# Kernel optimization log

Measured on AMD Instinct MI355X. Metric: run time of the kernel, lower is better.

Reference implementation:

```python
import jax, jax.numpy as jnp
import numpy as np

COMMITMENT_COST = 0.25


def setup_inputs() -> dict:
    key = jax.random.key(0)
    kx, ke = jax.random.split(key)
    x = jax.random.normal(kx, (16, 2048, 256), dtype=jnp.float32)
    embedding = jax.random.normal(ke, (4096, 256), dtype=jnp.float32)
    return {"x": x, "embedding": embedding}


def reference(x, embedding):
    # x: [B, T, D], embedding: [M, D]. Eval-mode VQ-EMA forward (no buffer updates).
    B, T, D = x.shape
    M = embedding.shape[0]
    x_flat = x.reshape(-1, D)  # [N, D], N = B*T

    distances = (
        jnp.sum(embedding * embedding, axis=1)[None, :]
        + jnp.sum(x_flat * x_flat, axis=1, keepdims=True)
        - 2.0 * (x_flat @ embedding.T)
    )
    indices = jnp.argmin(distances.astype(jnp.float32), axis=-1)  # [N]
    quantized = embedding[indices].reshape(x.shape)  # gather lookup, [B, T, D]

    # commitment loss, masked by nonpadding frames
    e_latent = (x - jax.lax.stop_gradient(quantized)) ** 2  # mse, reduction='none'
    nonpadding = (jnp.abs(x).sum(-1) > 0).astype(x.dtype)  # [B, T]
    e_latent_loss = (e_latent.mean(-1) * nonpadding).sum() / nonpadding.sum()
    loss = COMMITMENT_COST * e_latent_loss

    # straight-through estimator
    quantized_st = x + jax.lax.stop_gradient(quantized - x)

    # perplexity from code usage histogram (avoid materializing [N, M] one-hot)
    counts = jnp.zeros((M,), jnp.float32).at[indices].add(1.0)
    avg_probs = counts / indices.shape[0]
    perplexity = jnp.exp(-jnp.sum(avg_probs * jnp.log(avg_probs + 1e-10)))

    return quantized_st, loss, indices.reshape(B, T), perplexity
```

## Files before the change

### kernel.cpp

```cpp
#include <hip/hip_runtime.h>
#include <math.h>
#include <stdint.h>

#define D 256
#define N 32768
#define M 4096

#define LOSS_OFF 8388608
#define IDX_OFF  8388609
#define PERP_OFF 8421377

typedef _Float16 f16;
typedef _Float16 f16x8 __attribute__((ext_vector_type(8)));
typedef _Float16 f16x4 __attribute__((ext_vector_type(4)));
typedef float f32x4 __attribute__((ext_vector_type(4)));

#define WS_XH     0u
#define WS_XL     16777216u
#define WS_EH     33554432u
#define WS_EL     35651584u
#define WS_ENORM  37748736u
#define WS_COUNTS 37765120u
#define WS_IDX    37781504u
#define WS_CAND   37912576u
#define WS_LPART  38961152u
#define WS_NPART  38969344u
#define WS_NEEDED 38977536u
#define C_BLOCKS  2048

__device__ __forceinline__ void gload16(const void* g, void* l) {
    __builtin_amdgcn_global_load_lds(
        (const __attribute__((address_space(1))) uint32_t*)g,
        (__attribute__((address_space(3))) uint32_t*)l, 16, 0, 0);
}

__global__ __launch_bounds__(256) void init_kernel(const float* __restrict__ emb,
                                                   float* __restrict__ enorm,
                                                   unsigned* __restrict__ counts) {
    int tid = threadIdx.x;
    int lane = tid & 63;
    int wid = tid >> 6;
    int m = blockIdx.x * 4 + wid;
    const float4* e4 = (const float4*)(emb + (size_t)m * D);
    float4 v = e4[lane];
    float s = v.x * v.x + v.y * v.y + v.z * v.z + v.w * v.w;
    #pragma unroll
    for (int off = 32; off; off >>= 1) s += __shfl_xor(s, off);
    if (lane == 0) enorm[m] = s;
    int gid = blockIdx.x * 256 + tid;
    if (gid < M) counts[gid] = 0u;
}

__global__ __launch_bounds__(256) void convert_kernel(const float* __restrict__ s,
                                                      f16* __restrict__ dh,
                                                      f16* __restrict__ dl, int n4) {
    int i = blockIdx.x * 256 + threadIdx.x;
    if (i >= n4) return;
    float4 v = ((const float4*)s)[i];
    f16 h0 = (f16)v.x, h1 = (f16)v.y, h2 = (f16)v.z, h3 = (f16)v.w;
    f16 l0 = (f16)(v.x - (float)h0), l1 = (f16)(v.y - (float)h1);
    f16 l2 = (f16)(v.z - (float)h2), l3 = (f16)(v.w - (float)h3);
    f16x4 hv; hv[0] = h0; hv[1] = h1; hv[2] = h2; hv[3] = h3;
    f16x4 lv; lv[0] = l0; lv[1] = l1; lv[2] = l2; lv[3] = l3;
    *(f16x4*)(dh + (size_t)i * 4) = hv;
    *(f16x4*)(dl + (size_t)i * 4) = lv;
}

__global__ __launch_bounds__(256) void argmin_mfma(
    const f16* __restrict__ xh, const f16* __restrict__ xl,
    const f16* __restrict__ eh, const f16* __restrict__ el,
    const float* __restrict__ enorm, float2* __restrict__ cand)
{
    __shared__ f16 Als[2][128][64];
    __shared__ f16 Bls[2][128][64];
    __shared__ float2 msm[2][64];

    int tid = threadIdx.x;
    int lane = tid & 63;
    int wid = tid >> 6;
    int wr = wid >> 1, wc = wid & 1;
    int rb = blockIdx.x >> 2;
    int cs = blockIdx.x & 3;
    int row0 = rb * 128;

    int srow = lane >> 3;
    int sk = (((lane & 7) ^ srow) * 8);

    int rxor = lane & 7;

    float bestv[4][4];
    int bestc[4][4];
    #pragma unroll
    for (int i = 0; i < 4; ++i)
        #pragma unroll
        for (int r = 0; r < 4; ++r) { bestv[i][r] = 3.4e38f; bestc[i][r] = 0; }

    for (int ct = 0; ct < 8; ++ct) {
        int c0 = (cs * 8 + ct) * 128;
        f32x4 acc[4][4];
        #pragma unroll
        for (int i = 0; i < 4; ++i)
            #pragma unroll
            for (int j = 0; j < 4; ++j) acc[i][j] = (f32x4)0.0f;

        for (int kt = 0; kt < 4; ++kt) {
            int k0 = kt * 64;
            __syncthreads();
            #pragma unroll
            for (int q = 0; q < 4; ++q) {
                int ch = wid * 4 + q;
                int tr = ch * 8 + srow;
                size_t aoff = (size_t)(row0 + tr) * D + k0 + sk;
                size_t boff = (size_t)(c0 + tr) * D + k0 + sk;
                gload16(xh + aoff, (char*)&Als[0][0][0] + ch * 1024);
                gload16(xl + aoff, (char*)&Als[1][0][0] + ch * 1024);
                gload16(eh + boff, (char*)&Bls[0][0][0] + ch * 1024);
                gload16(el + boff, (char*)&Bls[1][0][0] + ch * 1024);
            }
            __syncthreads();

            #pragma unroll
            for (int ks = 0; ks < 2; ++ks) {
                int slot = ks * 4 + (lane >> 4);
                int sw = ((slot ^ rxor) * 8);
                int ar = wr * 64 + (lane & 15);
                int br = wc * 64 + (lane & 15);
                f16x8 ah[4], al[4], bh[4], bl[4];
                #pragma unroll
                for (int i = 0; i < 4; ++i) {
                    ah[i] = *(const f16x8*)&Als[0][ar + i * 16][sw];
                    al[i] = *(const f16x8*)&Als[1][ar + i * 16][sw];
                }
                #pragma unroll
                for (int j = 0; j < 4; ++j) {
                    bh[j] = *(const f16x8*)&Bls[0][br + j * 16][sw];
                    bl[j] = *(const f16x8*)&Bls[1][br + j * 16][sw];
                }
                #pragma unroll
                for (int i = 0; i < 4; ++i)
                    #pragma unroll
                    for (int j = 0; j < 4; ++j)
                        acc[i][j] = __builtin_amdgcn_mfma_f32_16x16x32_f16(
                            ah[i], bh[j], acc[i][j], 0, 0, 0);
                #pragma unroll
                for (int i = 0; i < 4; ++i)
                    #pragma unroll
                    for (int j = 0; j < 4; ++j)
                        acc[i][j] = __builtin_amdgcn_mfma_f32_16x16x32_f16(
                            ah[i], bl[j], acc[i][j], 0, 0, 0);
                #pragma unroll
                for (int i = 0; i < 4; ++i)
                    #pragma unroll
                    for (int j = 0; j < 4; ++j)
                        acc[i][j] = __builtin_amdgcn_mfma_f32_16x16x32_f16(
                            al[i], bh[j], acc[i][j], 0, 0, 0);
            }
        }
        float enj[4];
        #pragma unroll
        for (int j = 0; j < 4; ++j) enj[j] = enorm[c0 + wc * 64 + j * 16 + (lane & 15)];
        #pragma unroll
        for (int i = 0; i < 4; ++i)
            #pragma unroll
            for (int j = 0; j < 4; ++j) {
                int c = c0 + wc * 64 + j * 16 + (lane & 15);
                #pragma unroll
                for (int r = 0; r < 4; ++r) {
                    float s = enj[j] - 2.0f * acc[i][j][r];
                    if (s < bestv[i][r]) { bestv[i][r] = s; bestc[i][r] = c; }
                }
            }
    }

    float rv[4][4]; int rc[4][4];
    #pragma unroll
    for (int i = 0; i < 4; ++i)
        #pragma unroll
        for (int r = 0; r < 4; ++r) {
            float v = bestv[i][r]; int c = bestc[i][r];
            #pragma unroll
            for (int off = 8; off; off >>= 1) {
                float ov = __shfl_xor(v, off);
                int oc = __shfl_xor(c, off);
                if (ov < v || (ov == v && oc < c)) { v = ov; c = oc; }
            }
            rv[i][r] = v; rc[i][r] = c;
            if ((lane & 15) == 0 && wc == 1) {
                int rloc = i * 16 + (lane >> 4) * 4 + r;
                float2 p; p.x = v; p.y = __int_as_float(c);
                msm[wr][rloc] = p;
            }
        }
    __syncthreads();
    if (wc == 0 && (lane & 15) == 0) {
        #pragma unroll
        for (int i = 0; i < 4; ++i)
            #pragma unroll
            for (int r = 0; r < 4; ++r) {
                int rloc = i * 16 + (lane >> 4) * 4 + r;
                float v = rv[i][r]; int c = rc[i][r];
                float2 o = msm[wr][rloc];
                float ov = o.x; int oc = __float_as_int(o.y);
                if (ov < v || (ov == v && oc < c)) { v = ov; c = oc; }
                float2 p; p.x = v; p.y = __int_as_float(c);
                cand[(size_t)cs * N + row0 + wr * 64 + rloc] = p;
            }
    }
}

__global__ __launch_bounds__(256) void merge_kernel(const float2* __restrict__ cand,
                                                    unsigned* __restrict__ counts,
                                                    int* __restrict__ idx_out,
                                                    float* __restrict__ idx_f) {
    int row = blockIdx.x * 256 + threadIdx.x;
    float bv = 3.4e38f; int bc = 0;
    #pragma unroll
    for (int cs = 0; cs < 4; ++cs) {
        float2 p = cand[(size_t)cs * N + row];
        int c = __float_as_int(p.y);
        if (p.x < bv || (p.x == bv && c < bc)) { bv = p.x; bc = c; }
    }
    idx_out[row] = bc;
    idx_f[row] = (float)bc;
    atomicAdd(&counts[bc], 1u);
}

#define BR 64
#define BC 128
#define BK 64
__global__ __launch_bounds__(256) void argmin_fp32(
    const float* __restrict__ x, const float* __restrict__ emb,
    const float* __restrict__ enorm, unsigned* __restrict__ counts,
    int* __restrict__ idx_out, float* __restrict__ idx_f)
{
    __shared__ float xs[BR][65];
    __shared__ float es[BC][65];
    __shared__ float en_s[BC];
    int tid = threadIdx.x;
    int ty = tid >> 4, tx = tid & 15;
    int r0 = blockIdx.x * BR;
    float bestv[4]; int bestc[4];
    #pragma unroll
    for (int i = 0; i < 4; ++i) { bestv[i] = 3.4e38f; bestc[i] = 0; }
    for (int ct = 0; ct < M / BC; ++ct) {
        int c0 = ct * BC;
        float acc[4][8];
        #pragma unroll
        for (int i = 0; i < 4; ++i)
            #pragma unroll
            for (int j = 0; j < 8; ++j) acc[i][j] = 0.0f;
        for (int kt = 0; kt < D / BK; ++kt) {
            __syncthreads();
            #pragma unroll
            for (int p = 0; p < 4; ++p) {
                int l = p * 256 + tid, r = l >> 4, k4 = l & 15;
                float4 v = *(const float4*)(x + (size_t)(r0 + r) * D + kt * BK + k4 * 4);
                xs[r][k4 * 4] = v.x; xs[r][k4 * 4 + 1] = v.y;
                xs[r][k4 * 4 + 2] = v.z; xs[r][k4 * 4 + 3] = v.w;
            }
            #pragma unroll
            for (int p = 0; p < 8; ++p) {
                int l = p * 256 + tid, r = l >> 4, k4 = l & 15;
                float4 v = *(const float4*)(emb + (size_t)(c0 + r) * D + kt * BK + k4 * 4);
                es[r][k4 * 4] = v.x; es[r][k4 * 4 + 1] = v.y;
                es[r][k4 * 4 + 2] = v.z; es[r][k4 * 4 + 3] = v.w;
            }
            if (kt == 0 && tid < BC) en_s[tid] = enorm[c0 + tid];
            __syncthreads();
            #pragma unroll 8
            for (int k = 0; k < BK; ++k) {
                float xv[4], ev[8];
                #pragma unroll
                for (int i = 0; i < 4; ++i) xv[i] = xs[ty + 16 * i][k];
                #pragma unroll
                for (int j = 0; j < 8; ++j) ev[j] = es[tx + 16 * j][k];
                #pragma unroll
                for (int i = 0; i < 4; ++i)
                    #pragma unroll
                    for (int j = 0; j < 8; ++j)
                        acc[i][j] = fmaf(xv[i], ev[j], acc[i][j]);
            }
        }
        #pragma unroll
        for (int i = 0; i < 4; ++i)
            #pragma unroll
            for (int j = 0; j < 8; ++j) {
                int c = c0 + tx + 16 * j;
                float s = en_s[tx + 16 * j] - 2.0f * acc[i][j];
                if (s < bestv[i]) { bestv[i] = s; bestc[i] = c; }
            }
    }
    #pragma unroll
    for (int i = 0; i < 4; ++i) {
        float v = bestv[i]; int c = bestc[i];
        #pragma unroll
        for (int off = 8; off; off >>= 1) {
            float ov = __shfl_xor(v, off, 16);
            int oc = __shfl_xor(c, off, 16);
            if (ov < v || (ov == v && oc < c)) { v = ov; c = oc; }
        }
        if (tx == 0) {
            int row = r0 + ty + 16 * i;
            idx_out[row] = c; idx_f[row] = (float)c;
            atomicAdd(&counts[c], 1u);
        }
    }
}

__global__ __launch_bounds__(256) void gather_kernel(
    const float* __restrict__ x, const float* __restrict__ emb,
    const int* __restrict__ idx, float* __restrict__ out,
    float* __restrict__ lpart, float* __restrict__ npart)
{
    int tid = threadIdx.x, lane = tid & 63, wid = tid >> 6;
    __shared__ float ls[4], ns[4];
    double lacc = 0.0, nacc = 0.0;
    for (int it = 0; it < 4; ++it) {
        int row = (blockIdx.x * 4 + wid) + it * (C_BLOCKS * 4);
        int c = idx[row];
        float4 xv = *(const float4*)(x + (size_t)row * D + lane * 4);
        float4 qv = *(const float4*)(emb + (size_t)c * D + lane * 4);
        float4 o;
        o.x = xv.x + (qv.x - xv.x); o.y = xv.y + (qv.y - xv.y);
        o.z = xv.z + (qv.z - xv.z); o.w = xv.w + (qv.w - xv.w);
        *(float4*)(out + (size_t)row * D + lane * 4) = o;
        float dx = xv.x - qv.x, dy = xv.y - qv.y, dz = xv.z - qv.z, dw = xv.w - qv.w;
        float ss = dx * dx + dy * dy + dz * dz + dw * dw;
        float sa = fabsf(xv.x) + fabsf(xv.y) + fabsf(xv.z) + fabsf(xv.w);
        #pragma unroll
        for (int off = 32; off; off >>= 1) {
            ss += __shfl_xor(ss, off);
            sa += __shfl_xor(sa, off);
        }
        if (sa > 0.0f) { lacc += (double)ss * (1.0 / 256.0); nacc += 1.0; }
    }
    if (lane == 0) { ls[wid] = (float)lacc; ns[wid] = (float)nacc; }
    __syncthreads();
    if (tid == 0) {
        lpart[blockIdx.x] = ls[0] + ls[1] + ls[2] + ls[3];
        npart[blockIdx.x] = ns[0] + ns[1] + ns[2] + ns[3];
    }
}

__global__ __launch_bounds__(256) void finalize_kernel(
    const unsigned* __restrict__ counts, const float* __restrict__ lpart,
    const float* __restrict__ npart, float* __restrict__ out)
{
    __shared__ double sd[256];
    __shared__ double sl[256];
    __shared__ double sn[256];
    int tid = threadIdx.x;
    double t = 0.0;
    for (int i = tid; i < M; i += 256) {
        double p = (double)counts[i] * (1.0 / 32768.0);
        t += p * log(p + 1e-10);
    }
    sd[tid] = t;
    double ln = 0.0, nn = 0.0;
    for (int i = tid; i < C_BLOCKS; i += 256) { ln += lpart[i]; nn += npart[i]; }
    sl[tid] = ln; sn[tid] = nn;
    __syncthreads();
    for (int s = 128; s; s >>= 1) {
        if (tid < s) { sd[tid] += sd[tid + s]; sl[tid] += sl[tid + s]; sn[tid] += sn[tid + s]; }
        __syncthreads();
    }
    if (tid == 0) {
        out[PERP_OFF] = (float)exp(-sd[0]);
        out[LOSS_OFF] = (float)(0.25 * sl[0] / sn[0]);
    }
}

extern "C" void kernel_launch(void* const* d_in, const int* in_sizes, int n_in,
                              void* d_out, int out_size, void* d_ws, size_t ws_size,
                              hipStream_t stream) {
    const float* x = (const float*)d_in[0];
    const float* emb = (const float*)d_in[1];
    float* out = (float*)d_out;
    char* ws = (char*)d_ws;

    float* enorm = (float*)(ws + WS_ENORM);
    unsigned* counts = (unsigned*)(ws + WS_COUNTS);
    int* idx = (int*)(ws + WS_IDX);
    float* lpart = (float*)(ws + WS_LPART);
    float* npart = (float*)(ws + WS_NPART);

    if (ws_size >= (size_t)WS_NEEDED) {
        f16* xh = (f16*)(ws + WS_XH);
        f16* xl = (f16*)(ws + WS_XL);
        f16* eh = (f16*)(ws + WS_EH);
        f16* el = (f16*)(ws + WS_EL);
        float2* cand = (float2*)(ws + WS_CAND);

        init_kernel<<<M / 4, 256, 0, stream>>>(emb, enorm, counts);
        convert_kernel<<<(N * D / 4) / 256, 256, 0, stream>>>(x, xh, xl, N * D / 4);
        convert_kernel<<<(M * D / 4) / 256, 256, 0, stream>>>(emb, eh, el, M * D / 4);
        argmin_mfma<<<1024, 256, 0, stream>>>(xh, xl, eh, el, enorm, cand);
        merge_kernel<<<N / 256, 256, 0, stream>>>(cand, counts, idx, out + IDX_OFF);
    } else {
        enorm = (float*)(ws + 0);
        counts = (unsigned*)(ws + 16384);
        idx = (int*)(ws + 32768);
        lpart = (float*)(ws + 163840);
        npart = (float*)(ws + 172032);
        init_kernel<<<M / 4, 256, 0, stream>>>(emb, enorm, counts);
        argmin_fp32<<<N / BR, 256, 0, stream>>>(x, emb, enorm, counts, idx, out + IDX_OFF);
    }
    gather_kernel<<<C_BLOCKS, 256, 0, stream>>>(x, emb, idx, out, lpart, npart);
    finalize_kernel<<<1, 256, 0, stream>>>(counts, lpart, npart, out);
}
```

Measured before the change: 340.6 us.

## Keep x-high tile resident in LDS, x-low in registers, double-buffer codebook loads

The argmin GEMM kernel now runs 512 threads per block with 8 waves. It loads the full 128x256 fp16 x-high tile into LDS once and keeps the x-low fragments in registers for the whole block. Only codebook hi/lo chunks are streamed, through a double-buffered LDS ring with a prefetch of the next k-chunk. Block-to-tile mapping is also remapped so blocks sharing a codebook slice run together. This removes repeated x reloads and gives load/compute overlap, at the cost of 96KB dynamic LDS and higher register pressure, which limit occupancy.

Result: faster. 322.6 us (-5.3%).

```diff
diff --git a/kernel.cpp b/kernel.cpp
--- a/kernel.cpp
+++ b/kernel.cpp
@@ -33,6 +33,8 @@
         (const __attribute__((address_space(1))) uint32_t*)g,
         (__attribute__((address_space(3))) uint32_t*)l, 16, 0, 0);
 }
+
+#define MFMA16(a, b, c) __builtin_amdgcn_mfma_f32_16x16x32_f16((a), (b), (c), 0, 0, 0)
 
 __global__ __launch_bounds__(256) void init_kernel(const float* __restrict__ emb,
                                                    float* __restrict__ enorm,
@@ -66,101 +68,131 @@
     *(f16x4*)(dl + (size_t)i * 4) = lv;
 }
 
-__global__ __launch_bounds__(256) void argmin_mfma(
+__global__ __launch_bounds__(512) void argmin_xp(
     const f16* __restrict__ xh, const f16* __restrict__ xl,
     const f16* __restrict__ eh, const f16* __restrict__ el,
     const float* __restrict__ enorm, float2* __restrict__ cand)
 {
-    __shared__ f16 Als[2][128][64];
-    __shared__ f16 Bls[2][128][64];
-    __shared__ float2 msm[2][64];
+    extern __shared__ char smem[];
+    f16* Xh = (f16*)smem;
+    f16* EBa = (f16*)(smem + 65536);
+    float2 (*msm)[32] = (float2(*)[32])(smem + 65536);
 
     int tid = threadIdx.x;
     int lane = tid & 63;
     int wid = tid >> 6;
-    int wr = wid >> 1, wc = wid & 1;
-    int rb = blockIdx.x >> 2;
-    int cs = blockIdx.x & 3;
+    int wr = wid >> 1;
+    int wc = wid & 1;
+    int b = blockIdx.x;
+    int rb = (b & 7) * 32 + (b >> 5);
+    int cs = (b >> 3) & 3;
     int row0 = rb * 128;
-
-    int srow = lane >> 3;
-    int sk = (((lane & 7) ^ srow) * 8);
-
     int rxor = lane & 7;
 
-    float bestv[4][4];
-    int bestc[4][4];
-    #pragma unroll
-    for (int i = 0; i < 4; ++i)
+    {
+        int srow = lane >> 5, lslot = lane & 31;
+        #pragma unroll
+        for (int q = 0; q < 8; ++q) {
+            int ch = wid * 8 + q;
+            int row = ch * 2 + srow;
+            int ss = lslot ^ (row & 7);
+            gload16(xh + (size_t)(row0 + row) * D + ss * 8, smem + ch * 1024);
+        }
+    }
+    {
+        int srow = lane >> 3, lslot = lane & 7;
+        int c0 = cs * 1024;
+        #pragma unroll
+        for (int q = 0; q < 2; ++q) {
+            int ch = wid * 2 + q;
+            int row = ch * 8 + srow;
+            int ss = lslot ^ (row & 7);
+            const f16* src = (ss < 4) ? eh : el;
+            gload16(src + (size_t)(c0 + row) * D + (ss & 3) * 8,
+                    smem + 65536 + ch * 1024);
+        }
+    }
+    f16x8 xlr[2][8];
+    #pragma unroll
+    for (int i = 0; i < 2; ++i) {
+        int row = row0 + wr * 32 + i * 16 + (lane & 15);
+        #pragma unroll
+        for (int kc = 0; kc < 8; ++kc)
+            xlr[i][kc] = *(const f16x8*)(xl + (size_t)row * D + kc * 32 + (lane >> 4) * 8);
+    }
+    __syncthreads();
+
+    float bestv[2][4];
+    int bestc[2][4];
+    #pragma unroll
+    for (int i = 0; i < 2; ++i)
         #pragma unroll
         for (int r = 0; r < 4; ++r) { bestv[i][r] = 3.4e38f; bestc[i][r] = 0; }
 
     for (int ct = 0; ct < 8; ++ct) {
         int c0 = (cs * 8 + ct) * 128;
-        f32x4 acc[4][4];
-        #pragma unroll
-        for (int i = 0; i < 4; ++i)
+        f32x4 acc[2][4];
+        #pragma unroll
+        for (int i = 0; i < 2; ++i)
             #pragma unroll
             for (int j = 0; j < 4; ++j) acc[i][j] = (f32x4)0.0f;
 
-        for (int kt = 0; kt < 4; ++kt) {
-            int k0 = kt * 64;
-            __syncthreads();
-            #pragma unroll
-            for (int q = 0; q < 4; ++q) {
-                int ch = wid * 4 + q;
-                int tr = ch * 8 + srow;
-                size_t aoff = (size_t)(row0 + tr) * D + k0 + sk;
-                size_t boff = (size_t)(c0 + tr) * D + k0 + sk;
-                gload16(xh + aoff, (char*)&Als[0][0][0] + ch * 1024);
-                gload16(xl + aoff, (char*)&Als[1][0][0] + ch * 1024);
-                gload16(eh + boff, (char*)&Bls[0][0][0] + ch * 1024);
-                gload16(el + boff, (char*)&Bls[1][0][0] + ch * 1024);
-            }
-            __syncthreads();
-
-            #pragma unroll
-            for (int ks = 0; ks < 2; ++ks) {
-                int slot = ks * 4 + (lane >> 4);
-                int sw = ((slot ^ rxor) * 8);
-                int ar = wr * 64 + (lane & 15);
-                int br = wc * 64 + (lane & 15);
-                f16x8 ah[4], al[4], bh[4], bl[4];
-                #pragma unroll
-                for (int i = 0; i < 4; ++i) {
-                    ah[i] = *(const f16x8*)&Als[0][ar + i * 16][sw];
-                    al[i] = *(const f16x8*)&Als[1][ar + i * 16][sw];
+        #pragma unroll
+        for (int kc = 0; kc < 8; ++kc) {
+            if (ct * 8 + kc < 63) {
+                int t1 = ct * 8 + kc + 1;
+                int ct1 = t1 >> 3, kc1 = t1 & 7, d1 = t1 & 1;
+                int c01 = (cs * 8 + ct1) * 128;
+                int srow = lane >> 3, lslot = lane & 7;
+                #pragma unroll
+                for (int q = 0; q < 2; ++q) {
+                    int ch = wid * 2 + q;
+                    int row = ch * 8 + srow;
+                    int ss = lslot ^ (row & 7);
+                    const f16* src = (ss < 4) ? eh : el;
+                    gload16(src + (size_t)(c01 + row) * D + kc1 * 32 + (ss & 3) * 8,
+                            smem + 65536 + d1 * 16384 + ch * 1024);
                 }
+            }
+            {
+                const f16* EB = EBa + (kc & 1) * 8192;
+                f16x8 ah[2], bh[4], bl[4];
+                #pragma unroll
+                for (int i = 0; i < 2; ++i) {
+                    int row = wr * 32 + i * 16 + (lane & 15);
+                    int sl = (kc * 4 + (lane >> 4)) ^ rxor;
+                    ah[i] = *(const f16x8*)(Xh + row * 256 + sl * 8);
+                }
                 #pragma unroll
                 for (int j = 0; j < 4; ++j) {
-                    bh[j] = *(const f16x8*)&Bls[0][br + j * 16][sw];
-                    bl[j] = *(const f16x8*)&Bls[1][br + j * 16][sw];
+                    int row = wc * 64 + j * 16 + (lane & 15);
+                    const f16* ebr = EB + row * 64;
+                    bh[j] = *(const f16x8*)(ebr + (((lane >> 4)) ^ rxor) * 8);
+                    bl[j] = *(const f16x8*)(ebr + ((4 + (lane >> 4)) ^ rxor) * 8);
                 }
                 #pragma unroll
-                for (int i = 0; i < 4; ++i)
+                for (int i = 0; i < 2; ++i)
                     #pragma unroll
                     for (int j = 0; j < 4; ++j)
-                        acc[i][j] = __builtin_amdgcn_mfma_f32_16x16x32_f16(
-                            ah[i], bh[j], acc[i][j], 0, 0, 0);
-                #pragma unroll
-                for (int i = 0; i < 4; ++i)
+                        acc[i][j] = MFMA16(ah[i], bh[j], acc[i][j]);
+                #pragma unroll
+                for (int i = 0; i < 2; ++i)
                     #pragma unroll
                     for (int j = 0; j < 4; ++j)
-                        acc[i][j] = __builtin_amdgcn_mfma_f32_16x16x32_f16(
-                            ah[i], bl[j], acc[i][j], 0, 0, 0);
-                #pragma unroll
-                for (int i = 0; i < 4; ++i)
+                        acc[i][j] = MFMA16(ah[i], bl[j], acc[i][j]);
+                #pragma unroll
+                for (int i = 0; i < 2; ++i)
                     #pragma unroll
                     for (int j = 0; j < 4; ++j)
-                        acc[i][j] = __builtin_amdgcn_mfma_f32_16x16x32_f16(
-                            al[i], bh[j], acc[i][j], 0, 0, 0);
-            }
+                        acc[i][j] = MFMA16(xlr[i][kc], bh[j], acc[i][j]);
+            }
+            __syncthreads();
         }
         float enj[4];
         #pragma unroll
         for (int j = 0; j < 4; ++j) enj[j] = enorm[c0 + wc * 64 + j * 16 + (lane & 15)];
         #pragma unroll
-        for (int i = 0; i < 4; ++i)
+        for (int i = 0; i < 2; ++i)
             #pragma unroll
             for (int j = 0; j < 4; ++j) {
                 int c = c0 + wc * 64 + j * 16 + (lane & 15);
@@ -172,9 +204,9 @@
             }
     }
 
-    float rv[4][4]; int rc[4][4];
-    #pragma unroll
-    for (int i = 0; i < 4; ++i)
+    float rv[2][4]; int rc[2][4];
+    #pragma unroll
+    for (int i = 0; i < 2; ++i)
         #pragma unroll
         for (int r = 0; r < 4; ++r) {
             float v = bestv[i][r]; int c = bestc[i][r];
@@ -194,7 +226,7 @@
     __syncthreads();
     if (wc == 0 && (lane & 15) == 0) {
         #pragma unroll
-        for (int i = 0; i < 4; ++i)
+        for (int i = 0; i < 2; ++i)
             #pragma unroll
             for (int r = 0; r < 4; ++r) {
                 int rloc = i * 16 + (lane >> 4) * 4 + r;
@@ -203,7 +235,7 @@
                 float ov = o.x; int oc = __float_as_int(o.y);
                 if (ov < v || (ov == v && oc < c)) { v = ov; c = oc; }
                 float2 p; p.x = v; p.y = __int_as_float(c);
-                cand[(size_t)cs * N + row0 + wr * 64 + rloc] = p;
+                cand[(size_t)cs * N + row0 + wr * 32 + rloc] = p;
             }
     }
 }
@@ -394,7 +426,7 @@
         init_kernel<<<M / 4, 256, 0, stream>>>(emb, enorm, counts);
         convert_kernel<<<(N * D / 4) / 256, 256, 0, stream>>>(x, xh, xl, N * D / 4);
         convert_kernel<<<(M * D / 4) / 256, 256, 0, stream>>>(emb, eh, el, M * D / 4);
-        argmin_mfma<<<1024, 256, 0, stream>>>(xh, xl, eh, el, enorm, cand);
+        argmin_xp<<<1024, 512, 98304, stream>>>(xh, xl, eh, el, enorm, cand);
         merge_kernel<<<N / 256, 256, 0, stream>>>(cand, counts, idx, out + IDX_OFF);
     } else {
         enorm = (float*)(ws + 0);
```
